# Optimization experiments

Measured on AMD Instinct MI355X. Metric: run time of the kernel, lower is better.

The kernel has to match this reference:

```python
import jax, jax.numpy as jnp
import numpy as np
import math

L, D_T, D, NL, NH, FFN, C, B = 24, 1024, 256, 12, 4, 1024, 2, 2048
HD = D // NH


def _layernorm(x, g, b, eps=1e-5):
    m = jnp.mean(x, axis=-1, keepdims=True)
    v = jnp.mean(jnp.square(x - m), axis=-1, keepdims=True)
    return (x - m) * jax.lax.rsqrt(v + eps) * g + b


def _rotate_half(x):
    x1, x2 = jnp.split(x, 2, axis=-1)
    return jnp.concatenate([-x2, x1], axis=-1)


def setup_inputs() -> dict:
    key = jax.random.key(0)
    ks = iter(jax.random.split(key, 64))
    n = lambda shape, s=0.02: jax.random.normal(next(ks), shape, dtype=jnp.float32) * s
    inp = {}
    inp['teacher_cls'] = jax.random.normal(next(ks), (B, L, D_T), dtype=jnp.float32)
    # input LN + projection
    inp['in_ln_g'] = jnp.ones((D_T,), jnp.float32); inp['in_ln_b'] = jnp.zeros((D_T,), jnp.float32)
    inp['proj_w'] = n((D, D_T)); inp['proj_b'] = jnp.zeros((D,), jnp.float32)
    # RoPE caches (buffers)
    inv_freq = 1.0 / (10000.0 ** (np.arange(0, D, 2, dtype=np.float32) / D))
    t = np.arange(L, dtype=np.float32)
    freqs = np.einsum('i,j->ij', t, inv_freq)
    emb = np.concatenate([freqs, freqs], axis=-1)
    inp['cos_cached'] = jnp.asarray(np.cos(emb)[None])  # [1,L,D]
    inp['sin_cached'] = jnp.asarray(np.sin(emb)[None])
    inp['pre_ln_g'] = jnp.ones((D,), jnp.float32); inp['pre_ln_b'] = jnp.zeros((D,), jnp.float32)
    # stacked transformer layer params [NL, ...]
    inp['l_ln1_g'] = jnp.ones((NL, D), jnp.float32); inp['l_ln1_b'] = jnp.zeros((NL, D), jnp.float32)
    inp['l_inw'] = n((NL, 3 * D, D)); inp['l_inb'] = jnp.zeros((NL, 3 * D), jnp.float32)
    inp['l_outw'] = n((NL, D, D)); inp['l_outb'] = jnp.zeros((NL, D), jnp.float32)
    inp['l_ln2_g'] = jnp.ones((NL, D), jnp.float32); inp['l_ln2_b'] = jnp.zeros((NL, D), jnp.float32)
    inp['l_w12'] = n((NL, 2 * FFN, D)); inp['l_b12'] = jnp.zeros((NL, 2 * FFN), jnp.float32)
    inp['l_w3'] = n((NL, D, FFN)); inp['l_b3'] = jnp.zeros((NL, D), jnp.float32)
    inp['post_ln_g'] = jnp.ones((D,), jnp.float32); inp['post_ln_b'] = jnp.zeros((D,), jnp.float32)
    # entropy gate
    inp['eg_w1'] = n((L, D, 8), 0.01); inp['eg_b1'] = jnp.zeros((L, 8), jnp.float32)
    inp['eg_w2'] = n((L, 8, 1), 0.01); inp['eg_b2'] = jnp.zeros((L, 1), jnp.float32)
    # per-position heads (stacked)
    inp['halt_w'] = n((L, D + 1)); inp['halt_b'] = jnp.full((L,), -4.0, jnp.float32)
    inp['cls_w'] = n((L, C, D)); inp['cls_b'] = jnp.zeros((L, C), jnp.float32)
    return inp


def _mha(x, inw, inb, outw, outb, mask):
    Bb, Ll, Dd = x.shape
    qkv = x @ inw.T + inb                              # [B,L,3D]
    q, k, v = jnp.split(qkv, 3, axis=-1)
    def heads(t):
        return t.reshape(Bb, Ll, NH, HD).transpose(0, 2, 1, 3)  # [B,H,L,hd]
    q, k, v = heads(q), heads(k), heads(v)
    scores = jnp.einsum('bhqd,bhkd->bhqk', q, k) / math.sqrt(HD)
    scores = jnp.where(mask, -jnp.inf, scores)
    attn = jax.nn.softmax(scores, axis=-1)
    o = jnp.einsum('bhqk,bhkd->bhqd', attn, v)
    o = o.transpose(0, 2, 1, 3).reshape(Bb, Ll, Dd)
    return o @ outw.T + outb


def reference(teacher_cls, in_ln_g, in_ln_b, proj_w, proj_b, cos_cached, sin_cached,
              pre_ln_g, pre_ln_b, l_ln1_g, l_ln1_b, l_inw, l_inb, l_outw, l_outb,
              l_ln2_g, l_ln2_b, l_w12, l_b12, l_w3, l_b3, post_ln_g, post_ln_b,
              eg_w1, eg_b1, eg_w2, eg_b2, halt_w, halt_b, cls_w, cls_b):
    x = _layernorm(teacher_cls, in_ln_g, in_ln_b)
    x = x @ proj_w.T + proj_b                          # [B,L,D]
    x = x * cos_cached + _rotate_half(x) * sin_cached  # RoPE
    z = _layernorm(x, pre_ln_g, pre_ln_b)
    mask = jnp.triu(jnp.ones((L, L), bool), 1)         # causal
    for i in range(NL):
        xn = _layernorm(z, l_ln1_g[i], l_ln1_b[i])
        z = z + _mha(xn, l_inw[i], l_inb[i], l_outw[i], l_outb[i], mask)
        xn = _layernorm(z, l_ln2_g[i], l_ln2_b[i])
        w12_out = xn @ l_w12[i].T + l_b12[i]           # [B,L,2*FFN]
        x1, x2 = jnp.split(w12_out, 2, axis=-1)
        hidden = jax.nn.silu(x1) * x2
        z = z + hidden @ l_w3[i].T + l_b3[i]
    z = _layernorm(z, post_ln_g, post_ln_b)
    # batched per-position classifier heads
    class_logits = jnp.einsum('bld,lcd->blc', z, cls_w) + cls_b   # [B,L,C]
    log_probs = jax.nn.log_softmax(class_logits, axis=-1)
    probs = jnp.exp(log_probs)
    probs_safe = jnp.clip(probs, 1e-10, 1.0)
    ent = -jnp.sum(probs_safe * jnp.log(probs_safe), axis=-1, keepdims=True)
    ent_norm = jnp.clip(ent / math.log(C), 0.0, 1.0)              # [B,L,1]
    # entropy gate
    h = jnp.tanh(jnp.einsum('bld,ldh->blh', z, eg_w1) + eg_b1)
    gate = jax.nn.sigmoid(jnp.einsum('blh,lho->blo', h, eg_w2) + eg_b2)
    gated = ent_norm * gate                                        # [B,L,1]
    # batched per-position halting heads
    combined = jnp.concatenate([z, gated], axis=-1)                # [B,L,D+1]
    halting_logits = jnp.einsum('bld,ld->bl', combined, halt_w) + halt_b
    return (halting_logits, class_logits, z)
```

## Files before the change

### kernel.cpp

```cpp
#include <hip/hip_runtime.h>
#include <hip/hip_bf16.h>
#include <math.h>

#define L_SEQ 24
#define DT 1024
#define DM 256
#define NLAYER 12
#define NHEAD 4
#define HDIM 64
#define FFND 1024
#define NCLS 2
#define NBATCH 2048
#define NTOK (NBATCH*L_SEQ)

typedef float f32x4 __attribute__((ext_vector_type(4)));
typedef __bf16 bf16x4 __attribute__((ext_vector_type(4)));
typedef __bf16 bf16x8 __attribute__((ext_vector_type(8)));

#define GLDS16(gp, lp) __builtin_amdgcn_global_load_lds((const __attribute__((address_space(1))) void*)(gp), (__attribute__((address_space(3))) void*)(lp), 16, 0, 0)

__device__ inline float wred_sum(float v){
#pragma unroll
  for (int o = 32; o > 0; o >>= 1) v += __shfl_xor(v, o);
  return v;
}
__device__ inline float wred_max(float v){
#pragma unroll
  for (int o = 32; o > 0; o >>= 1) v = fmaxf(v, __shfl_xor(v, o));
  return v;
}

__global__ void cvt_bf16_kernel(const float* __restrict__ in, __bf16* __restrict__ out, int n4){
  int i = blockIdx.x * blockDim.x + threadIdx.x;
  int stride = gridDim.x * blockDim.x;
  for (; i < n4; i += stride){
    float4 v = ((const float4*)in)[i];
    bf16x4 o;
    o[0] = (__bf16)v.x; o[1] = (__bf16)v.y; o[2] = (__bf16)v.z; o[3] = (__bf16)v.w;
    ((bf16x4*)out)[i] = o;
  }
}

__global__ __launch_bounds__(256) void ln1024_kernel(
    const float* __restrict__ in, const float* __restrict__ g, const float* __restrict__ bb,
    __bf16* __restrict__ out){
  int row = blockIdx.x;
  int tid = threadIdx.x, wid = tid >> 6, lane = tid & 63;
  float4 x = ((const float4*)(in + (size_t)row*DT))[tid];
  float s = x.x + x.y + x.z + x.w;
  float q = x.x*x.x + x.y*x.y + x.z*x.z + x.w*x.w;
  s = wred_sum(s); q = wred_sum(q);
  __shared__ float red[8];
  if (lane == 0){ red[wid] = s; red[4+wid] = q; }
  __syncthreads();
  s = red[0]+red[1]+red[2]+red[3];
  q = red[4]+red[5]+red[6]+red[7];
  float mean = s * (1.f/DT);
  float rstd = rsqrtf(q*(1.f/DT) - mean*mean + 1e-5f);
  float4 gv = ((const float4*)g)[tid], bv = ((const float4*)bb)[tid];
  bf16x4 o;
  o[0] = (__bf16)((x.x-mean)*rstd*gv.x + bv.x);
  o[1] = (__bf16)((x.y-mean)*rstd*gv.y + bv.y);
  o[2] = (__bf16)((x.z-mean)*rstd*gv.z + bv.z);
  o[3] = (__bf16)((x.w-mean)*rstd*gv.w + bv.w);
  ((bf16x4*)(out + (size_t)row*DT))[tid] = o;
}

__global__ __launch_bounds__(256) void ln256_kernel(
    const float* __restrict__ in, const float* __restrict__ g, const float* __restrict__ bb,
    __bf16* __restrict__ outb, float* __restrict__ outf){
  int row = blockIdx.x*4 + (threadIdx.x >> 6);
  int lane = threadIdx.x & 63;
  float4 x = ((const float4*)(in + (size_t)row*DM))[lane];
  float s = wred_sum(x.x + x.y + x.z + x.w);
  float q = wred_sum(x.x*x.x + x.y*x.y + x.z*x.z + x.w*x.w);
  float mean = s * (1.f/DM);
  float rstd = rsqrtf(q*(1.f/DM) - mean*mean + 1e-5f);
  float4 gv = ((const float4*)g)[lane], bv = ((const float4*)bb)[lane];
  float4 y;
  y.x = (x.x-mean)*rstd*gv.x + bv.x;
  y.y = (x.y-mean)*rstd*gv.y + bv.y;
  y.z = (x.z-mean)*rstd*gv.z + bv.z;
  y.w = (x.w-mean)*rstd*gv.w + bv.w;
  if (outb){
    bf16x4 o; o[0]=(__bf16)y.x; o[1]=(__bf16)y.y; o[2]=(__bf16)y.z; o[3]=(__bf16)y.w;
    ((bf16x4*)(outb + (size_t)row*DM))[lane] = o;
  }
  if (outf) ((float4*)(outf + (size_t)row*DM))[lane] = y;
}

__global__ __launch_bounds__(256) void rope_preln_kernel(
    float* __restrict__ z, const float* __restrict__ cosc, const float* __restrict__ sinc,
    const float* __restrict__ g, const float* __restrict__ bb){
  int row = blockIdx.x*4 + (threadIdx.x >> 6);
  int lane = threadIdx.x & 63;
  int l = row % L_SEQ;
  float4 x = ((const float4*)(z + (size_t)row*DM))[lane];
  float4 p;
  p.x = __shfl_xor(x.x, 32); p.y = __shfl_xor(x.y, 32);
  p.z = __shfl_xor(x.z, 32); p.w = __shfl_xor(x.w, 32);
  float sgn = (lane < 32) ? -1.f : 1.f;
  float4 c = ((const float4*)(cosc + l*DM))[lane];
  float4 sn = ((const float4*)(sinc + l*DM))[lane];
  float4 xr;
  xr.x = x.x*c.x + sgn*p.x*sn.x;
  xr.y = x.y*c.y + sgn*p.y*sn.y;
  xr.z = x.z*c.z + sgn*p.z*sn.z;
  xr.w = x.w*c.w + sgn*p.w*sn.w;
  float s = wred_sum(xr.x + xr.y + xr.z + xr.w);
  float q = wred_sum(xr.x*xr.x + xr.y*xr.y + xr.z*xr.z + xr.w*xr.w);
  float mean = s * (1.f/DM);
  float rstd = rsqrtf(q*(1.f/DM) - mean*mean + 1e-5f);
  float4 gv = ((const float4*)g)[lane], bv = ((const float4*)bb)[lane];
  float4 y;
  y.x = (xr.x-mean)*rstd*gv.x + bv.x;
  y.y = (xr.y-mean)*rstd*gv.y + bv.y;
  y.z = (xr.z-mean)*rstd*gv.z + bv.z;
  y.w = (xr.w-mean)*rstd*gv.w + bv.w;
  ((float4*)(z + (size_t)row*DM))[lane] = y;
}

template<int MODE>
__global__ __launch_bounds__(256) void gemm_kernel(
    const __bf16* __restrict__ A, const __bf16* __restrict__ W,
    const float* __restrict__ bias,
    float* __restrict__ Cf, __bf16* __restrict__ Cb,
    int N, int K, int nt){
  __shared__ __align__(16) __bf16 As[128*32];
  __shared__ __align__(16) __bf16 Bs[128*32];
  int bm = blockIdx.x / nt, bn = blockIdx.x % nt;
  int tid = threadIdx.x, wid = tid >> 6, lane = tid & 63;
  int wr = wid >> 1, wc = wid & 1;
  f32x4 acc[4][4] = {};
  const __bf16* ga = A + (size_t)(bm*128 + wid*16 + (lane>>2))*K + (lane&3)*8;
  const __bf16* gb = W + (size_t)(bn*128 + wid*16 + (lane>>2))*K + (lane&3)*8;
  for (int k0 = 0; k0 < K; k0 += 32){
    GLDS16(ga,            &As[wid*512]);
    GLDS16(ga + (size_t)64*K, &As[2048 + wid*512]);
    GLDS16(gb,            &Bs[wid*512]);
    GLDS16(gb + (size_t)64*K, &Bs[2048 + wid*512]);
    ga += 32; gb += 32;
    __syncthreads();
    bf16x8 af[4], bfr[4];
    int rk = (lane >> 4) << 3;
    int ra = (wr << 6) + (lane & 15);
    int rb = (wc << 6) + (lane & 15);
#pragma unroll
    for (int i = 0; i < 4; i++){
      af[i]  = *(const bf16x8*)&As[(ra + i*16)*32 + rk];
      bfr[i] = *(const bf16x8*)&Bs[(rb + i*16)*32 + rk];
    }
#pragma unroll
    for (int mi = 0; mi < 4; mi++)
#pragma unroll
      for (int ni = 0; ni < 4; ni++)
        acc[mi][ni] = __builtin_amdgcn_mfma_f32_16x16x32_bf16(af[mi], bfr[ni], acc[mi][ni], 0, 0, 0);
    __syncthreads();
  }
  int colbase = bn*128 + wc*64 + (lane & 15);
  int rowbase = bm*128 + wr*64 + ((lane >> 4) << 2);
#pragma unroll
  for (int mi = 0; mi < 4; mi++){
#pragma unroll
    for (int ni = 0; ni < 4; ni++){
      int col = colbase + ni*16;
      float bv = bias[col];
      int m0 = rowbase + mi*16;
#pragma unroll
      for (int r = 0; r < 4; r++){
        float v = acc[mi][ni][r] + bv;
        size_t idx = (size_t)(m0 + r)*N + col;
        if (MODE == 0) Cf[idx] = v;
        else if (MODE == 1) Cb[idx] = (__bf16)v;
        else Cf[idx] += v;
      }
    }
  }
}

__global__ __launch_bounds__(256) void gemm_glu_kernel(
    const __bf16* __restrict__ A, const __bf16* __restrict__ W12,
    const float* __restrict__ bias, __bf16* __restrict__ H){
  __shared__ __align__(16) __bf16 As[128*32];
  __shared__ __align__(16) __bf16 B1s[128*32];
  __shared__ __align__(16) __bf16 B2s[128*32];
  const int K = 256;
  int bm = blockIdx.x >> 3, bn = blockIdx.x & 7;
  int tid = threadIdx.x, wid = tid >> 6, lane = tid & 63;
  int wr = wid >> 1, wc = wid & 1;
  f32x4 acc1[4][4] = {}, acc2[4][4] = {};
  const __bf16* ga  = A   + (size_t)(bm*128 + wid*16 + (lane>>2))*K + (lane&3)*8;
  const __bf16* gb1 = W12 + (size_t)(bn*128 + wid*16 + (lane>>2))*K + (lane&3)*8;
  const __bf16* gb2 = gb1 + (size_t)1024*K;
  for (int k0 = 0; k0 < K; k0 += 32){
    GLDS16(ga,             &As[wid*512]);
    GLDS16(ga + 64*K,      &As[2048 + wid*512]);
    GLDS16(gb1,            &B1s[wid*512]);
    GLDS16(gb1 + 64*K,     &B1s[2048 + wid*512]);
    GLDS16(gb2,            &B2s[wid*512]);
    GLDS16(gb2 + 64*K,     &B2s[2048 + wid*512]);
    ga += 32; gb1 += 32; gb2 += 32;
    __syncthreads();
    bf16x8 af[4], b1f[4], b2f[4];
    int rk = (lane >> 4) << 3;
    int ra = (wr << 6) + (lane & 15);
    int rb = (wc << 6) + (lane & 15);
#pragma unroll
    for (int i = 0; i < 4; i++){
      af[i]  = *(const bf16x8*)&As[(ra + i*16)*32 + rk];
      b1f[i] = *(const bf16x8*)&B1s[(rb + i*16)*32 + rk];
      b2f[i] = *(const bf16x8*)&B2s[(rb + i*16)*32 + rk];
    }
#pragma unroll
    for (int mi = 0; mi < 4; mi++)
#pragma unroll
      for (int ni = 0; ni < 4; ni++){
        acc1[mi][ni] = __builtin_amdgcn_mfma_f32_16x16x32_bf16(af[mi], b1f[ni], acc1[mi][ni], 0, 0, 0);
        acc2[mi][ni] = __builtin_amdgcn_mfma_f32_16x16x32_bf16(af[mi], b2f[ni], acc2[mi][ni], 0, 0, 0);
      }
    __syncthreads();
  }
  int colbase = bn*128 + wc*64 + (lane & 15);
  int rowbase = bm*128 + wr*64 + ((lane >> 4) << 2);
#pragma unroll
  for (int mi = 0; mi < 4; mi++)
#pragma unroll
    for (int ni = 0; ni < 4; ni++){
      int col = colbase + ni*16;
      float b1 = bias[col], b2 = bias[1024 + col];
      int m0 = rowbase + mi*16;
#pragma unroll
      for (int r = 0; r < 4; r++){
        float v1 = acc1[mi][ni][r] + b1;
        float v2 = acc2[mi][ni][r] + b2;
        float sig = 1.f/(1.f + __expf(-v1));
        H[(size_t)(m0 + r)*FFND + col] = (__bf16)(v1*sig*v2);
      }
    }
}

__global__ __launch_bounds__(256) void attn_kernel(const __bf16* __restrict__ qkv, __bf16* __restrict__ ob){
  int b = blockIdx.x;
  int h = threadIdx.x >> 6, lane = threadIdx.x & 63;
  __shared__ __align__(16) __bf16 Qs[NHEAD][L_SEQ][HDIM];
  __shared__ __align__(16) __bf16 Ks[NHEAD][L_SEQ][HDIM];
  __shared__ float Ps[NHEAD][L_SEQ][L_SEQ];
  const __bf16* base = qkv + (size_t)b*L_SEQ*768;
  float V[L_SEQ];
#pragma unroll
  for (int t = 0; t < L_SEQ; t++){
    int sw = lane ^ ((t & 7) << 3);
    Qs[h][t][sw] = base[t*768 + h*64 + lane];
    Ks[h][t][sw] = base[t*768 + 256 + h*64 + lane];
    V[t] = (float)base[t*768 + 512 + h*64 + lane];
  }
  __syncthreads();
  for (int p = lane; p < L_SEQ*L_SEQ; p += 64){
    int q = p / L_SEQ, k = p - q*L_SEQ;
    if (k <= q){
      int qx = (q & 7) << 3, kx = (k & 7) << 3;
      const __bf16* qr = Qs[h][q];
      const __bf16* kr = Ks[h][k];
      float s = 0.f;
#pragma unroll
      for (int d = 0; d < 64; d += 4){
        bf16x4 qa = *(const bf16x4*)(qr + (d ^ qx));
        bf16x4 ka = *(const bf16x4*)(kr + (d ^ kx));
        s += (float)qa[0]*(float)ka[0] + (float)qa[1]*(float)ka[1]
           + (float)qa[2]*(float)ka[2] + (float)qa[3]*(float)ka[3];
      }
      Ps[h][q][k] = s * 0.125f;
    }
  }
  __syncthreads();
  for (int q = 0; q < L_SEQ; q++){
    float v = (lane <= q) ? Ps[h][q][lane] : -1e30f;
    float mx = wred_max(v);
    float e = (lane <= q) ? __expf(v - mx) : 0.f;
    float sm = wred_sum(e);
    if (lane < L_SEQ) Ps[h][q][lane] = e / sm;
  }
  __syncthreads();
  for (int q = 0; q < L_SEQ; q++){
    float o = 0.f;
    for (int k = 0; k <= q; k++) o += Ps[h][q][k] * V[k];
    ob[((size_t)b*L_SEQ + q)*DM + h*64 + lane] = (__bf16)o;
  }
}

__global__ __launch_bounds__(256) void heads_kernel(
    const float* __restrict__ z,
    const float* __restrict__ cls_w, const float* __restrict__ cls_b,
    const float* __restrict__ eg_w1, const float* __restrict__ eg_b1,
    const float* __restrict__ eg_w2, const float* __restrict__ eg_b2,
    const float* __restrict__ halt_w, const float* __restrict__ halt_b,
    float* __restrict__ halt_out, float* __restrict__ cls_out){
  int m = blockIdx.x*4 + (threadIdx.x >> 6);
  int lane = threadIdx.x & 63;
  int l = m % L_SEQ;
  float4 zv = ((const float4*)(z + (size_t)m*DM))[lane];
  float4 w0 = ((const float4*)(cls_w + ((size_t)l*2 + 0)*DM))[lane];
  float4 w1 = ((const float4*)(cls_w + ((size_t)l*2 + 1)*DM))[lane];
  float c0 = wred_sum(zv.x*w0.x + zv.y*w0.y + zv.z*w0.z + zv.w*w0.w) + cls_b[l*2 + 0];
  float c1 = wred_sum(zv.x*w1.x + zv.y*w1.y + zv.z*w1.z + zv.w*w1.w) + cls_b[l*2 + 1];
  float mx = fmaxf(c0, c1);
  float e0 = __expf(c0 - mx), e1 = __expf(c1 - mx);
  float inv = 1.f/(e0 + e1);
  float p0 = fminf(fmaxf(e0*inv, 1e-10f), 1.f);
  float p1 = fminf(fmaxf(e1*inv, 1e-10f), 1.f);
  float ent = -(p0*__logf(p0) + p1*__logf(p1));
  float entn = fminf(fmaxf(ent * 1.44269504f, 0.f), 1.f);
  const float4* wg = (const float4*)(eg_w1 + ((size_t)l*DM + 4*lane)*8);
  float hacc[8] = {};
#pragma unroll
  for (int dd = 0; dd < 4; dd++){
    float zd = (dd==0) ? zv.x : (dd==1) ? zv.y : (dd==2) ? zv.z : zv.w;
    float4 a = wg[dd*2], b = wg[dd*2 + 1];
    hacc[0] += zd*a.x; hacc[1] += zd*a.y; hacc[2] += zd*a.z; hacc[3] += zd*a.w;
    hacc[4] += zd*b.x; hacc[5] += zd*b.y; hacc[6] += zd*b.z; hacc[7] += zd*b.w;
  }
  float gin = 0.f;
#pragma unroll
  for (int j = 0; j < 8; j++){
    float hj = wred_sum(hacc[j]);
    hj = tanhf(hj + eg_b1[l*8 + j]);
    gin += hj * eg_w2[l*8 + j];
  }
  gin += eg_b2[l];
  float gate = 1.f/(1.f + __expf(-gin));
  float gated = entn * gate;
  const float* hw = halt_w + (size_t)l*257;
  float hp = zv.x*hw[4*lane] + zv.y*hw[4*lane+1] + zv.z*hw[4*lane+2] + zv.w*hw[4*lane+3];
  float hl = wred_sum(hp) + gated*hw[256] + halt_b[l];
  if (lane == 0) halt_out[m] = hl;
  if (lane < 2) cls_out[(size_t)m*2 + lane] = lane ? c1 : c0;
}

extern "C" void kernel_launch(void* const* d_in, const int* in_sizes, int n_in,
                              void* d_out, int out_size, void* d_ws, size_t ws_size,
                              hipStream_t stream){
  const float* teacher = (const float*)d_in[0];
  const float* in_ln_g = (const float*)d_in[1];
  const float* in_ln_b = (const float*)d_in[2];
  const float* proj_w  = (const float*)d_in[3];
  const float* proj_b  = (const float*)d_in[4];
  const float* cosc    = (const float*)d_in[5];
  const float* sinc    = (const float*)d_in[6];
  const float* pre_g   = (const float*)d_in[7];
  const float* pre_b   = (const float*)d_in[8];
  const float* l_ln1_g = (const float*)d_in[9];
  const float* l_ln1_b = (const float*)d_in[10];
  const float* l_inw   = (const float*)d_in[11];
  const float* l_inb   = (const float*)d_in[12];
  const float* l_outw  = (const float*)d_in[13];
  const float* l_outb  = (const float*)d_in[14];
  const float* l_ln2_g = (const float*)d_in[15];
  const float* l_ln2_b = (const float*)d_in[16];
  const float* l_w12   = (const float*)d_in[17];
  const float* l_b12   = (const float*)d_in[18];
  const float* l_w3    = (const float*)d_in[19];
  const float* l_b3    = (const float*)d_in[20];
  const float* post_g  = (const float*)d_in[21];
  const float* post_b  = (const float*)d_in[22];
  const float* eg_w1   = (const float*)d_in[23];
  const float* eg_b1   = (const float*)d_in[24];
  const float* eg_w2   = (const float*)d_in[25];
  const float* eg_b2   = (const float*)d_in[26];
  const float* halt_w  = (const float*)d_in[27];
  const float* halt_b  = (const float*)d_in[28];
  const float* cls_w   = (const float*)d_in[29];
  const float* cls_b   = (const float*)d_in[30];

  float* out = (float*)d_out;
  float* halt_out = out;
  float* cls_out  = out + NTOK;
  float* z_out    = out + NTOK + (size_t)NTOK*NCLS;

  char* ws = (char*)d_ws;
  size_t off = 0;
  auto alloc = [&](size_t bytes){ void* p = ws + off; off += (bytes + 255) & ~(size_t)255; return p; };
  float*  zbuf = (float*) alloc((size_t)NTOK*DM*4);
  __bf16* xnb  = (__bf16*)alloc((size_t)NTOK*DM*2);
  __bf16* qkvb = (__bf16*)alloc((size_t)NTOK*768*2);
  __bf16* obuf = (__bf16*)alloc((size_t)NTOK*DM*2);
  __bf16* bigb = (__bf16*)alloc((size_t)NTOK*1024*2);
  __bf16* w_proj = (__bf16*)alloc((size_t)262144*2);
  __bf16* w_in   = (__bf16*)alloc((size_t)2359296*2);
  __bf16* w_out  = (__bf16*)alloc((size_t)786432*2);
  __bf16* w_12   = (__bf16*)alloc((size_t)6291456*2);
  __bf16* w_3    = (__bf16*)alloc((size_t)3145728*2);

  cvt_bf16_kernel<<<256, 256, 0, stream>>>(proj_w, w_proj, 262144/4);
  cvt_bf16_kernel<<<1024, 256, 0, stream>>>(l_inw, w_in, 2359296/4);
  cvt_bf16_kernel<<<512, 256, 0, stream>>>(l_outw, w_out, 786432/4);
  cvt_bf16_kernel<<<2048, 256, 0, stream>>>(l_w12, w_12, 6291456/4);
  cvt_bf16_kernel<<<1024, 256, 0, stream>>>(l_w3, w_3, 3145728/4);

  ln1024_kernel<<<NTOK, 256, 0, stream>>>(teacher, in_ln_g, in_ln_b, bigb);
  gemm_kernel<0><<<384*2, 256, 0, stream>>>(bigb, w_proj, proj_b, zbuf, nullptr, 256, 1024, 2);
  rope_preln_kernel<<<NTOK/4, 256, 0, stream>>>(zbuf, cosc, sinc, pre_g, pre_b);

  for (int i = 0; i < NLAYER; i++){
    ln256_kernel<<<NTOK/4, 256, 0, stream>>>(zbuf, l_ln1_g + i*256, l_ln1_b + i*256, xnb, nullptr);
    gemm_kernel<1><<<384*6, 256, 0, stream>>>(xnb, w_in + (size_t)i*768*256, l_inb + i*768, nullptr, qkvb, 768, 256, 6);
    attn_kernel<<<NBATCH, 256, 0, stream>>>(qkvb, obuf);
    gemm_kernel<2><<<384*2, 256, 0, stream>>>(obuf, w_out + (size_t)i*256*256, l_outb + i*256, zbuf, nullptr, 256, 256, 2);
    ln256_kernel<<<NTOK/4, 256, 0, stream>>>(zbuf, l_ln2_g + i*256, l_ln2_b + i*256, xnb, nullptr);
    gemm_glu_kernel<<<384*8, 256, 0, stream>>>(xnb, w_12 + (size_t)i*2048*256, l_b12 + i*2048, bigb);
    gemm_kernel<2><<<384*2, 256, 0, stream>>>(bigb, w_3 + (size_t)i*256*1024, l_b3 + i*256, zbuf, nullptr, 256, 1024, 2);
  }

  ln256_kernel<<<NTOK/4, 256, 0, stream>>>(zbuf, post_g, post_b, nullptr, z_out);
  heads_kernel<<<NTOK/4, 256, 0, stream>>>(z_out, cls_w, cls_b, eg_w1, eg_b1, eg_w2, eg_b2,
                                           halt_w, halt_b, halt_out, cls_out);
}
```

Baseline: 4.628 ms.

## Fuse residual add and LayerNorm into GEMM epilogues, widen K tiles with swizzled LDS

Removes the standalone ln256 kernels by computing the residual add plus the next LayerNorm inside a new full-row (64x256) GEMM epilogue for the out-proj and w3 GEMMs. The first layer's LN1 moves into the rope/pre-LN kernel. All GEMMs now stage K=64 per iteration with an XOR-swizzled LDS layout to reduce bank conflicts and halve barrier count. The cost is fewer, larger blocks for the LN-fused GEMMs (768 blocks, each reloading the full 256-row weight tile) and more LDS per block, which lowers occupancy.

```diff
diff --git a/kernel.cpp b/kernel.cpp
--- a/kernel.cpp
+++ b/kernel.cpp
@@ -28,6 +28,18 @@
 #pragma unroll
   for (int o = 32; o > 0; o >>= 1) v = fmaxf(v, __shfl_xor(v, o));
   return v;
+}
+
+__device__ __forceinline__ void stage8(const __bf16* __restrict__ gtile, int ldk, int k0,
+                                       __bf16* lds, int r8, int lane){
+  int rloc = (r8 << 3) + (lane >> 3);
+  int c = (lane & 7) ^ (rloc & 7);
+  GLDS16(gtile + (size_t)rloc*ldk + k0 + c*8, lds + (r8 << 9));
+}
+
+__device__ __forceinline__ bf16x8 ldsfrag(const __bf16* tile, int row, int kk, int lane){
+  int c = ((kk << 2) + (lane >> 4)) ^ (row & 7);
+  return *(const bf16x8*)(tile + (row << 6) + (c << 3));
 }
 
 __global__ void cvt_bf16_kernel(const float* __restrict__ in, __bf16* __restrict__ out, int n4){
@@ -66,32 +78,10 @@
   ((bf16x4*)(out + (size_t)row*DT))[tid] = o;
 }
 
-__global__ __launch_bounds__(256) void ln256_kernel(
-    const float* __restrict__ in, const float* __restrict__ g, const float* __restrict__ bb,
-    __bf16* __restrict__ outb, float* __restrict__ outf){
-  int row = blockIdx.x*4 + (threadIdx.x >> 6);
-  int lane = threadIdx.x & 63;
-  float4 x = ((const float4*)(in + (size_t)row*DM))[lane];
-  float s = wred_sum(x.x + x.y + x.z + x.w);
-  float q = wred_sum(x.x*x.x + x.y*x.y + x.z*x.z + x.w*x.w);
-  float mean = s * (1.f/DM);
-  float rstd = rsqrtf(q*(1.f/DM) - mean*mean + 1e-5f);
-  float4 gv = ((const float4*)g)[lane], bv = ((const float4*)bb)[lane];
-  float4 y;
-  y.x = (x.x-mean)*rstd*gv.x + bv.x;
-  y.y = (x.y-mean)*rstd*gv.y + bv.y;
-  y.z = (x.z-mean)*rstd*gv.z + bv.z;
-  y.w = (x.w-mean)*rstd*gv.w + bv.w;
-  if (outb){
-    bf16x4 o; o[0]=(__bf16)y.x; o[1]=(__bf16)y.y; o[2]=(__bf16)y.z; o[3]=(__bf16)y.w;
-    ((bf16x4*)(outb + (size_t)row*DM))[lane] = o;
-  }
-  if (outf) ((float4*)(outf + (size_t)row*DM))[lane] = y;
-}
-
 __global__ __launch_bounds__(256) void rope_preln_kernel(
     float* __restrict__ z, const float* __restrict__ cosc, const float* __restrict__ sinc,
-    const float* __restrict__ g, const float* __restrict__ bb){
+    const float* __restrict__ g, const float* __restrict__ bb,
+    const float* __restrict__ g1, const float* __restrict__ b1, __bf16* __restrict__ xnb){
   int row = blockIdx.x*4 + (threadIdx.x >> 6);
   int lane = threadIdx.x & 63;
   int l = row % L_SEQ;
@@ -118,43 +108,52 @@
   y.z = (xr.z-mean)*rstd*gv.z + bv.z;
   y.w = (xr.w-mean)*rstd*gv.w + bv.w;
   ((float4*)(z + (size_t)row*DM))[lane] = y;
+  float s2 = wred_sum(y.x + y.y + y.z + y.w);
+  float q2 = wred_sum(y.x*y.x + y.y*y.y + y.z*y.z + y.w*y.w);
+  float mean2 = s2 * (1.f/DM);
+  float rstd2 = rsqrtf(q2*(1.f/DM) - mean2*mean2 + 1e-5f);
+  float4 g1v = ((const float4*)g1)[lane], b1v = ((const float4*)b1)[lane];
+  bf16x4 o;
+  o[0] = (__bf16)((y.x-mean2)*rstd2*g1v.x + b1v.x);
+  o[1] = (__bf16)((y.y-mean2)*rstd2*g1v.y + b1v.y);
+  o[2] = (__bf16)((y.z-mean2)*rstd2*g1v.z + b1v.z);
+  o[3] = (__bf16)((y.w-mean2)*rstd2*g1v.w + b1v.w);
+  ((bf16x4*)(xnb + (size_t)row*DM))[lane] = o;
 }
 
 template<int MODE>
-__global__ __launch_bounds__(256) void gemm_kernel(
+__global__ __launch_bounds__(256) void gemm128_kernel(
     const __bf16* __restrict__ A, const __bf16* __restrict__ W,
     const float* __restrict__ bias,
     float* __restrict__ Cf, __bf16* __restrict__ Cb,
     int N, int K, int nt){
-  __shared__ __align__(16) __bf16 As[128*32];
-  __shared__ __align__(16) __bf16 Bs[128*32];
+  __shared__ __align__(16) __bf16 As[128*64];
+  __shared__ __align__(16) __bf16 Bs[128*64];
   int bm = blockIdx.x / nt, bn = blockIdx.x % nt;
   int tid = threadIdx.x, wid = tid >> 6, lane = tid & 63;
   int wr = wid >> 1, wc = wid & 1;
   f32x4 acc[4][4] = {};
-  const __bf16* ga = A + (size_t)(bm*128 + wid*16 + (lane>>2))*K + (lane&3)*8;
-  const __bf16* gb = W + (size_t)(bn*128 + wid*16 + (lane>>2))*K + (lane&3)*8;
-  for (int k0 = 0; k0 < K; k0 += 32){
-    GLDS16(ga,            &As[wid*512]);
-    GLDS16(ga + (size_t)64*K, &As[2048 + wid*512]);
-    GLDS16(gb,            &Bs[wid*512]);
-    GLDS16(gb + (size_t)64*K, &Bs[2048 + wid*512]);
-    ga += 32; gb += 32;
-    __syncthreads();
-    bf16x8 af[4], bfr[4];
-    int rk = (lane >> 4) << 3;
-    int ra = (wr << 6) + (lane & 15);
-    int rb = (wc << 6) + (lane & 15);
-#pragma unroll
-    for (int i = 0; i < 4; i++){
-      af[i]  = *(const bf16x8*)&As[(ra + i*16)*32 + rk];
-      bfr[i] = *(const bf16x8*)&Bs[(rb + i*16)*32 + rk];
-    }
-#pragma unroll
-    for (int mi = 0; mi < 4; mi++)
-#pragma unroll
-      for (int ni = 0; ni < 4; ni++)
-        acc[mi][ni] = __builtin_amdgcn_mfma_f32_16x16x32_bf16(af[mi], bfr[ni], acc[mi][ni], 0, 0, 0);
+  const __bf16* ga = A + (size_t)bm*128*K;
+  const __bf16* gb = W + (size_t)bn*128*K;
+  for (int k0 = 0; k0 < K; k0 += 64){
+#pragma unroll
+    for (int j = 0; j < 4; j++) stage8(ga, K, k0, As, wid*4 + j, lane);
+#pragma unroll
+    for (int j = 0; j < 4; j++) stage8(gb, K, k0, Bs, wid*4 + j, lane);
+    __syncthreads();
+#pragma unroll
+    for (int kk = 0; kk < 2; kk++){
+      bf16x8 af[4], bfr[4];
+#pragma unroll
+      for (int mi = 0; mi < 4; mi++) af[mi]  = ldsfrag(As, wr*64 + mi*16 + (lane&15), kk, lane);
+#pragma unroll
+      for (int ni = 0; ni < 4; ni++) bfr[ni] = ldsfrag(Bs, wc*64 + ni*16 + (lane&15), kk, lane);
+#pragma unroll
+      for (int mi = 0; mi < 4; mi++)
+#pragma unroll
+        for (int ni = 0; ni < 4; ni++)
+          acc[mi][ni] = __builtin_amdgcn_mfma_f32_16x16x32_bf16(af[mi], bfr[ni], acc[mi][ni], 0, 0, 0);
+    }
     __syncthreads();
   }
   int colbase = bn*128 + wc*64 + (lane & 15);
@@ -171,8 +170,7 @@
         float v = acc[mi][ni][r] + bv;
         size_t idx = (size_t)(m0 + r)*N + col;
         if (MODE == 0) Cf[idx] = v;
-        else if (MODE == 1) Cb[idx] = (__bf16)v;
-        else Cf[idx] += v;
+        else Cb[idx] = (__bf16)v;
       }
     }
   }
@@ -181,43 +179,43 @@
 __global__ __launch_bounds__(256) void gemm_glu_kernel(
     const __bf16* __restrict__ A, const __bf16* __restrict__ W12,
     const float* __restrict__ bias, __bf16* __restrict__ H){
-  __shared__ __align__(16) __bf16 As[128*32];
-  __shared__ __align__(16) __bf16 B1s[128*32];
-  __shared__ __align__(16) __bf16 B2s[128*32];
+  __shared__ __align__(16) __bf16 As[128*64];
+  __shared__ __align__(16) __bf16 B1s[128*64];
+  __shared__ __align__(16) __bf16 B2s[128*64];
   const int K = 256;
   int bm = blockIdx.x >> 3, bn = blockIdx.x & 7;
   int tid = threadIdx.x, wid = tid >> 6, lane = tid & 63;
   int wr = wid >> 1, wc = wid & 1;
   f32x4 acc1[4][4] = {}, acc2[4][4] = {};
-  const __bf16* ga  = A   + (size_t)(bm*128 + wid*16 + (lane>>2))*K + (lane&3)*8;
-  const __bf16* gb1 = W12 + (size_t)(bn*128 + wid*16 + (lane>>2))*K + (lane&3)*8;
+  const __bf16* ga  = A   + (size_t)bm*128*K;
+  const __bf16* gb1 = W12 + (size_t)bn*128*K;
   const __bf16* gb2 = gb1 + (size_t)1024*K;
-  for (int k0 = 0; k0 < K; k0 += 32){
-    GLDS16(ga,             &As[wid*512]);
-    GLDS16(ga + 64*K,      &As[2048 + wid*512]);
-    GLDS16(gb1,            &B1s[wid*512]);
-    GLDS16(gb1 + 64*K,     &B1s[2048 + wid*512]);
-    GLDS16(gb2,            &B2s[wid*512]);
-    GLDS16(gb2 + 64*K,     &B2s[2048 + wid*512]);
-    ga += 32; gb1 += 32; gb2 += 32;
-    __syncthreads();
-    bf16x8 af[4], b1f[4], b2f[4];
-    int rk = (lane >> 4) << 3;
-    int ra = (wr << 6) + (lane & 15);
-    int rb = (wc << 6) + (lane & 15);
-#pragma unroll
-    for (int i = 0; i < 4; i++){
-      af[i]  = *(const bf16x8*)&As[(ra + i*16)*32 + rk];
-      b1f[i] = *(const bf16x8*)&B1s[(rb + i*16)*32 + rk];
-      b2f[i] = *(const bf16x8*)&B2s[(rb + i*16)*32 + rk];
-    }
-#pragma unroll
-    for (int mi = 0; mi < 4; mi++)
+  for (int k0 = 0; k0 < K; k0 += 64){
+#pragma unroll
+    for (int j = 0; j < 4; j++) stage8(ga,  K, k0, As,  wid*4 + j, lane);
+#pragma unroll
+    for (int j = 0; j < 4; j++) stage8(gb1, K, k0, B1s, wid*4 + j, lane);
+#pragma unroll
+    for (int j = 0; j < 4; j++) stage8(gb2, K, k0, B2s, wid*4 + j, lane);
+    __syncthreads();
+#pragma unroll
+    for (int kk = 0; kk < 2; kk++){
+      bf16x8 af[4], b1f[4], b2f[4];
+#pragma unroll
+      for (int mi = 0; mi < 4; mi++) af[mi]  = ldsfrag(As,  wr*64 + mi*16 + (lane&15), kk, lane);
 #pragma unroll
       for (int ni = 0; ni < 4; ni++){
-        acc1[mi][ni] = __builtin_amdgcn_mfma_f32_16x16x32_bf16(af[mi], b1f[ni], acc1[mi][ni], 0, 0, 0);
-        acc2[mi][ni] = __builtin_amdgcn_mfma_f32_16x16x32_bf16(af[mi], b2f[ni], acc2[mi][ni], 0, 0, 0);
-      }
+        b1f[ni] = ldsfrag(B1s, wc*64 + ni*16 + (lane&15), kk, lane);
+        b2f[ni] = ldsfrag(B2s, wc*64 + ni*16 + (lane&15), kk, lane);
+      }
+#pragma unroll
+      for (int mi = 0; mi < 4; mi++)
+#pragma unroll
+        for (int ni = 0; ni < 4; ni++){
+          acc1[mi][ni] = __builtin_amdgcn_mfma_f32_16x16x32_bf16(af[mi], b1f[ni], acc1[mi][ni], 0, 0, 0);
+          acc2[mi][ni] = __builtin_amdgcn_mfma_f32_16x16x32_bf16(af[mi], b2f[ni], acc2[mi][ni], 0, 0, 0);
+        }
+    }
     __syncthreads();
   }
   int colbase = bn*128 + wc*64 + (lane & 15);
@@ -235,6 +233,86 @@
         float v2 = acc2[mi][ni][r] + b2;
         float sig = 1.f/(1.f + __expf(-v1));
         H[(size_t)(m0 + r)*FFND + col] = (__bf16)(v1*sig*v2);
+      }
+    }
+}
+
+__global__ __launch_bounds__(256) void gemm_ln_kernel(
+    const __bf16* __restrict__ A, const __bf16* __restrict__ W,
+    const float* __restrict__ bias, float* __restrict__ z,
+    const float* __restrict__ lng, const float* __restrict__ lnb,
+    __bf16* __restrict__ outb, float* __restrict__ outf, int K){
+  __shared__ __align__(16) __bf16 As[64*64];
+  __shared__ __align__(16) __bf16 Bs[256*64];
+  __shared__ float redS[64][4], redQ[64][4];
+  int bm = blockIdx.x;
+  int tid = threadIdx.x, wid = tid >> 6, lane = tid & 63;
+  const __bf16* ga = A + (size_t)bm*64*K;
+  f32x4 acc[4][4] = {};
+  for (int k0 = 0; k0 < K; k0 += 64){
+#pragma unroll
+    for (int j = 0; j < 2; j++) stage8(ga, K, k0, As, wid*2 + j, lane);
+#pragma unroll
+    for (int j = 0; j < 8; j++) stage8(W,  K, k0, Bs, wid*8 + j, lane);
+    __syncthreads();
+#pragma unroll
+    for (int kk = 0; kk < 2; kk++){
+      bf16x8 af[4], bfr[4];
+#pragma unroll
+      for (int mi = 0; mi < 4; mi++) af[mi]  = ldsfrag(As, mi*16 + (lane&15), kk, lane);
+#pragma unroll
+      for (int ni = 0; ni < 4; ni++) bfr[ni] = ldsfrag(Bs, wid*64 + ni*16 + (lane&15), kk, lane);
+#pragma unroll
+      for (int mi = 0; mi < 4; mi++)
+#pragma unroll
+        for (int ni = 0; ni < 4; ni++)
+          acc[mi][ni] = __builtin_amdgcn_mfma_f32_16x16x32_bf16(af[mi], bfr[ni], acc[mi][ni], 0, 0, 0);
+    }
+    __syncthreads();
+  }
+  int g = lane >> 4, li = lane & 15;
+  float sA[4][4] = {}, qA[4][4] = {};
+#pragma unroll
+  for (int mi = 0; mi < 4; mi++)
+#pragma unroll
+    for (int r = 0; r < 4; r++){
+      int rl = mi*16 + g*4 + r;
+      size_t rowg = (size_t)(bm*64 + rl)*DM;
+#pragma unroll
+      for (int ni = 0; ni < 4; ni++){
+        int col = wid*64 + ni*16 + li;
+        float v = acc[mi][ni][r] + bias[col] + z[rowg + col];
+        acc[mi][ni][r] = v;
+        z[rowg + col] = v;
+        sA[mi][r] += v; qA[mi][r] += v*v;
+      }
+    }
+#pragma unroll
+  for (int mi = 0; mi < 4; mi++)
+#pragma unroll
+    for (int r = 0; r < 4; r++){
+      float s = sA[mi][r], q = qA[mi][r];
+#pragma unroll
+      for (int off = 1; off < 16; off <<= 1){ s += __shfl_xor(s, off); q += __shfl_xor(q, off); }
+      if (li == 0){ redS[mi*16 + g*4 + r][wid] = s; redQ[mi*16 + g*4 + r][wid] = q; }
+    }
+  __syncthreads();
+#pragma unroll
+  for (int mi = 0; mi < 4; mi++)
+#pragma unroll
+    for (int r = 0; r < 4; r++){
+      int rl = mi*16 + g*4 + r;
+      float s = redS[rl][0] + redS[rl][1] + redS[rl][2] + redS[rl][3];
+      float q = redQ[rl][0] + redQ[rl][1] + redQ[rl][2] + redQ[rl][3];
+      float mean = s * (1.f/DM);
+      float rstd = rsqrtf(q*(1.f/DM) - mean*mean + 1e-5f);
+      size_t rowg = (size_t)(bm*64 + rl)*DM;
+#pragma unroll
+      for (int ni = 0; ni < 4; ni++){
+        int col = wid*64 + ni*16 + li;
+        float xn = (acc[mi][ni][r] - mean)*rstd*lng[col] + lnb[col];
+        if (outb) outb[rowg + col] = (__bf16)xn;
+        else      outf[rowg + col] = xn;
       }
     }
 }
@@ -397,20 +475,24 @@
   cvt_bf16_kernel<<<1024, 256, 0, stream>>>(l_w3, w_3, 3145728/4);
 
   ln1024_kernel<<<NTOK, 256, 0, stream>>>(teacher, in_ln_g, in_ln_b, bigb);
-  gemm_kernel<0><<<384*2, 256, 0, stream>>>(bigb, w_proj, proj_b, zbuf, nullptr, 256, 1024, 2);
-  rope_preln_kernel<<<NTOK/4, 256, 0, stream>>>(zbuf, cosc, sinc, pre_g, pre_b);
+  gemm128_kernel<0><<<384*2, 256, 0, stream>>>(bigb, w_proj, proj_b, zbuf, nullptr, 256, 1024, 2);
+  rope_preln_kernel<<<NTOK/4, 256, 0, stream>>>(zbuf, cosc, sinc, pre_g, pre_b, l_ln1_g, l_ln1_b, xnb);
 
   for (int i = 0; i < NLAYER; i++){
-    ln256_kernel<<<NTOK/4, 256, 0, stream>>>(zbuf, l_ln1_g + i*256, l_ln1_b + i*256, xnb, nullptr);
-    gemm_kernel<1><<<384*6, 256, 0, stream>>>(xnb, w_in + (size_t)i*768*256, l_inb + i*768, nullptr, qkvb, 768, 256, 6);
+    gemm128_kernel<1><<<384*6, 256, 0, stream>>>(xnb, w_in + (size_t)i*768*256, l_inb + i*768, nullptr, qkvb, 768, 256, 6);
     attn_kernel<<<NBATCH, 256, 0, stream>>>(qkvb, obuf);
-    gemm_kernel<2><<<384*2, 256, 0, stream>>>(obuf, w_out + (size_t)i*256*256, l_outb + i*256, zbuf, nullptr, 256, 256, 2);
-    ln256_kernel<<<NTOK/4, 256, 0, stream>>>(zbuf, l_ln2_g + i*256, l_ln2_b + i*256, xnb, nullptr);
+    gemm_ln_kernel<<<NTOK/64, 256, 0, stream>>>(obuf, w_out + (size_t)i*256*256, l_outb + i*256,
+                                                zbuf, l_ln2_g + i*256, l_ln2_b + i*256, xnb, nullptr, 256);
     gemm_glu_kernel<<<384*8, 256, 0, stream>>>(xnb, w_12 + (size_t)i*2048*256, l_b12 + i*2048, bigb);
-    gemm_kernel<2><<<384*2, 256, 0, stream>>>(bigb, w_3 + (size_t)i*256*1024, l_b3 + i*256, zbuf, nullptr, 256, 1024, 2);
-  }
-
-  ln256_kernel<<<NTOK/4, 256, 0, stream>>>(zbuf, post_g, post_b, nullptr, z_out);
+    bool last = (i == NLAYER-1);
+    gemm_ln_kernel<<<NTOK/64, 256, 0, stream>>>(bigb, w_3 + (size_t)i*256*1024, l_b3 + i*256,
+                                                zbuf,
+                                                last ? post_g : l_ln1_g + (i+1)*256,
+                                                last ? post_b : l_ln1_b + (i+1)*256,
+                                                last ? nullptr : xnb,
+                                                last ? z_out : nullptr, 1024);
+  }
+
   heads_kernel<<<NTOK/4, 256, 0, stream>>>(z_out, cls_w, cls_b, eg_w1, eg_b1, eg_w2, eg_b2,
                                            halt_w, halt_b, halt_out, cls_out);
 }
```

Measured after the change: 4.437 ms. -4.1%, faster.
